# Kernel tuning notes

Hardware: AMD Instinct MI355X
Metric: run time of the kernel (lower is better)

## Reference

```python
import jax, jax.numpy as jnp
import numpy as np

B, S, D = 4, 2048, 256


def setup_inputs() -> dict:
    key = jax.random.key(0)
    ks = jax.random.split(key, 8)
    context = jax.random.normal(ks[0], (B, S, D), dtype=jnp.float32)
    eos_mask = jax.random.randint(ks[1], (B, S, S), 0, 2, dtype=jnp.int32)
    prior = jax.random.uniform(ks[2], (B, S, S), dtype=jnp.float32)
    Wq = jax.random.normal(ks[3], (D, D), dtype=jnp.float32) * 0.02
    bq = jnp.zeros((D,), dtype=jnp.float32)
    Wk = jax.random.normal(ks[4], (D, D), dtype=jnp.float32) * 0.02
    bk = jnp.zeros((D,), dtype=jnp.float32)
    ln_a = jnp.ones((D,), dtype=jnp.float32)
    ln_b = jnp.zeros((D,), dtype=jnp.float32)
    return {"context": context, "prior": prior, "Wq": Wq, "bq": bq,
            "Wk": Wk, "bk": bk, "ln_a": ln_a, "ln_b": ln_b,
            "eos_mask": eos_mask}


def reference(context, prior, Wq, bq, Wk, bk, ln_a, ln_b, eos_mask):
    seq = context.shape[1]
    # LayerNorm (torch: unbiased std, eps added to std)
    mean = context.mean(axis=-1, keepdims=True)
    std = jnp.std(context, axis=-1, ddof=1, keepdims=True)
    x = ln_a * (context - mean) / (std + 1e-6) + ln_b

    idx = jnp.arange(seq)
    diff = idx[None, :] - idx[:, None]
    a = diff == 1                      # superdiagonal
    offdiag = jnp.abs(diff) == 1       # a + c (super + sub diagonal)
    eye = diff == 0                    # b
    tri = jnp.triu(jnp.ones((seq, seq), dtype=jnp.float32))

    # mask = eos_mask & (a + c)  (precedence: & binds looser than +)
    mask = jnp.bitwise_and(eos_mask, offdiag.astype(jnp.int32))

    # torch Linear: y = x @ W.T + b
    query = x @ Wq.T + bq
    key = x @ Wk.T + bk
    scores = jnp.einsum('bqd,bkd->bqk', query, key) / 256.0
    scores = jnp.where(mask == 0, -1e9, scores)
    neibor = jax.nn.softmax(scores, axis=-1)
    neibor = jnp.sqrt(neibor * neibor.transpose(0, 2, 1) + 1e-9)
    neibor = prior + (1.0 - prior) * neibor

    # log -> zero except superdiagonal -> triangular matmul -> exp
    t = jnp.where(a, jnp.log(neibor + 1e-9), 0.0) @ tri   # [B,S,S]
    g = jnp.exp(jnp.matmul(tri, t))                        # [B,S,S]
    strict_upper = jnp.logical_and(tri.astype(bool), jnp.logical_not(eye))
    g = jnp.where(strict_upper, g, 0.0)  # masked_fill(tri - b == 0, 0)
    g = g + g.transpose(0, 2, 1) + jnp.where(eye, neibor, 1e-9)
    return g
```

## Files before the change

kernel.cpp:

```cpp
#include <hip/hip_runtime.h>
#include <math.h>

#define SS 2048
#define DD 256
#define NB 4
#define NR (NB * SS)

__global__ __launch_bounds__(256) void prep_kernel(
    const float* __restrict__ Wq, const float* __restrict__ Wk,
    const float* __restrict__ bq, float* __restrict__ A, float* __restrict__ u) {
    int t = threadIdx.x;
    int d = blockIdx.x;
    if (d < DD) {
        float a0 = 0.f, a1 = 0.f, a2 = 0.f, a3 = 0.f;
        for (int i = 0; i < DD; i += 4) {
            a0 += Wq[(i + 0) * DD + d] * Wk[(i + 0) * DD + t];
            a1 += Wq[(i + 1) * DD + d] * Wk[(i + 1) * DD + t];
            a2 += Wq[(i + 2) * DD + d] * Wk[(i + 2) * DD + t];
            a3 += Wq[(i + 3) * DD + d] * Wk[(i + 3) * DD + t];
        }
        A[d * DD + t] = (a0 + a1) + (a2 + a3);
    } else {
        float a0 = 0.f, a1 = 0.f, a2 = 0.f, a3 = 0.f;
        for (int i = 0; i < DD; i += 4) {
            a0 += Wk[(i + 0) * DD + t] * bq[i + 0];
            a1 += Wk[(i + 1) * DD + t] * bq[i + 1];
            a2 += Wk[(i + 2) * DD + t] * bq[i + 2];
            a3 += Wk[(i + 3) * DD + t] * bq[i + 3];
        }
        u[t] = (a0 + a1) + (a2 + a3);
    }
}

#define ROWS 16
#define BK 32
#define XP 260
#define FMA4(accv, a, bv) \
    accv.x += (a) * bv.x; accv.y += (a) * bv.y; \
    accv.z += (a) * bv.z; accv.w += (a) * bv.w;

__global__ __launch_bounds__(256) void gemm_score_kernel(
    const float4* __restrict__ ctx4, const float4* __restrict__ ln_a4,
    const float4* __restrict__ ln_b4, const float* __restrict__ A,
    const float* __restrict__ u, const int* __restrict__ eos,
    float4* __restrict__ pvals) {
    __shared__ float Xn[ROWS + 2][XP];
    __shared__ float As[BK][256];
    int tid = threadIdx.x;
    int lane = tid & 63;
    int wave = tid >> 6;
    int row0 = blockIdx.x * ROWS;
    const float4* A4 = (const float4*)A;

    float4 ga = ln_a4[lane], gb = ln_b4[lane];
    for (int rr = wave; rr < ROWS + 2; rr += 4) {
        int g = row0 - 1 + rr;
        g = (g < 0) ? 0 : (g > NR - 1 ? NR - 1 : g);
        float4 v = ctx4[(size_t)g * 64 + lane];
        float s = v.x + v.y + v.z + v.w;
#pragma unroll
        for (int off = 32; off > 0; off >>= 1) s += __shfl_xor(s, off, 64);
        float mean = s * (1.0f / 256.0f);
        float4 dd = make_float4(v.x - mean, v.y - mean, v.z - mean, v.w - mean);
        float s2 = dd.x * dd.x + dd.y * dd.y + dd.z * dd.z + dd.w * dd.w;
#pragma unroll
        for (int off = 32; off > 0; off >>= 1) s2 += __shfl_xor(s2, off, 64);
        float inv = 1.0f / (sqrtf(s2 * (1.0f / 255.0f)) + 1e-6f);
        float* xr = &Xn[rr][lane * 4];
        xr[0] = ga.x * dd.x * inv + gb.x;
        xr[1] = ga.y * dd.y * inv + gb.y;
        xr[2] = ga.z * dd.z * inv + gb.z;
        xr[3] = ga.w * dd.w * inv + gb.w;
    }

    int tx = tid & 15, ty = tid >> 4;
    float4 acc[4] = {};
    const float* xr0 = &Xn[1 + ty][0];
    for (int k0 = 0; k0 < DD; k0 += BK) {
#pragma unroll
        for (int q = 0; q < 8; q++) {
            int f4 = q * 256 + tid;
            int k = f4 >> 6, c4 = f4 & 63;
            *(float4*)&As[k][c4 * 4] = A4[(size_t)(k0 + k) * 64 + c4];
        }
        __syncthreads();
#pragma unroll
        for (int k = 0; k < BK; k++) {
            float a0 = xr0[k0 + k];
            float4 b0 = *(const float4*)&As[k][tx * 4];
            float4 b1 = *(const float4*)&As[k][tx * 4 + 64];
            float4 b2 = *(const float4*)&As[k][tx * 4 + 128];
            float4 b3 = *(const float4*)&As[k][tx * 4 + 192];
            FMA4(acc[0], a0, b0) FMA4(acc[1], a0, b1)
            FMA4(acc[2], a0, b2) FMA4(acc[3], a0, b3)
        }
        __syncthreads();
    }

    const float4* u4 = (const float4*)u;
#pragma unroll
    for (int q = 0; q < 4; q++) {
        float4 uv = u4[q * 16 + tx];
        acc[q].x += uv.x; acc[q].y += uv.y; acc[q].z += uv.z; acc[q].w += uv.w;
    }
    {
        int li = 1 + ty;
        int r = row0 + ty;
        int s = r & (SS - 1), b = r >> 11;
        bool has_n = (s < SS - 1), has_p = (s > 0);
        float fn = has_n ? 1.0f : 0.0f, fp = has_p ? 1.0f : 0.0f;
        float partial = 0.0f;
#pragma unroll
        for (int q = 0; q < 4; q++) {
            int c = q * 64 + tx * 4;
            float wx = fn * Xn[li + 1][c + 0] - fp * Xn[li - 1][c + 0];
            float wy = fn * Xn[li + 1][c + 1] - fp * Xn[li - 1][c + 1];
            float wz = fn * Xn[li + 1][c + 2] - fp * Xn[li - 1][c + 2];
            float ww = fn * Xn[li + 1][c + 3] - fp * Xn[li - 1][c + 3];
            partial += acc[q].x * wx + acc[q].y * wy
                     + acc[q].z * wz + acc[q].w * ww;
        }
#pragma unroll
        for (int off = 8; off > 0; off >>= 1) partial += __shfl_xor(partial, off, 64);
        if (tx == 0) {
            size_t base = (size_t)b * SS * SS + (size_t)s * SS;
            bool mn = has_n && (eos[base + s + 1] != 0);
            bool mp = has_p && (eos[base + s - 1] != 0);
            float pn, pp, pd;
            if (mn && mp) {
                float d = partial * (1.0f / 256.0f);
                pn = 1.0f / (1.0f + __expf(-d));
                pp = 1.0f - pn;
                pd = 0.0f;
            } else if (mn) { pn = 1.0f; pp = 0.0f; pd = 0.0f; }
            else if (mp)   { pn = 0.0f; pp = 1.0f; pd = 0.0f; }
            else           { pn = pp = pd = (1.0f / 2048.0f); }
            pvals[r] = make_float4(pn, pp, pd, 0.0f);
        }
    }
}

__global__ __launch_bounds__(256) void scan_kernel(
    const float4* __restrict__ pvals, const float* __restrict__ prior,
    float* __restrict__ P) {
    int b = blockIdx.x, t = threadIdx.x;
    int base_s = t * 8;
    double loc[8];
    double run = 0.0;
#pragma unroll
    for (int i = 0; i < 8; i++) {
        loc[i] = run;
        int s = base_s + i;
        float lv = 0.0f;
        if (s < SS - 1) {
            int r = b * SS + s;
            float4 pv = pvals[r];
            float4 pv1 = pvals[r + 1];
            float ns = sqrtf(pv.x * pv1.y + 1e-9f);
            float pr = prior[(size_t)b * SS * SS + (size_t)s * SS + s + 1];
            float neib = pr + (1.0f - pr) * ns;
            lv = logf(neib + 1e-9f);
        }
        run += (double)lv;
    }
    int lane = t & 63, wave = t >> 6;
    double v = run;
#pragma unroll
    for (int off = 1; off < 64; off <<= 1) {
        double uu = __shfl_up(v, off, 64);
        if (lane >= off) v += uu;
    }
    __shared__ double wsum[4];
    if (lane == 63) wsum[wave] = v;
    __syncthreads();
    double woff = 0.0;
    for (int w = 0; w < wave; w++) woff += wsum[w];
    double texcl = woff + (v - run);
#pragma unroll
    for (int i = 0; i < 8; i++)
        P[b * SS + base_s + i] = (float)(texcl + loc[i]);
}

__global__ __launch_bounds__(256) void fill_kernel(
    const float* __restrict__ P, const float4* __restrict__ pvals,
    const float* __restrict__ prior, float* __restrict__ out) {
    int blk = blockIdx.x;
    int i = blk & (SS - 1), b = blk >> 11;
    int t = threadIdx.x;
    __shared__ float shPi, shDv;
    if (t == 0) {
        shPi = P[blk];
        float pd = pvals[blk].z;
        float prd = prior[(size_t)b * SS * SS + (size_t)i * SS + i];
        shDv = prd + (1.0f - prd) * sqrtf(pd * pd + 1e-9f);
    }
    __syncthreads();
    float Pi = shPi, dv = shDv;
    const float* Pb = P + b * SS;
    size_t outbase = (size_t)blk * SS;
    float4 pj0 = *(const float4*)(Pb + t * 8);
    float4 pj1 = *(const float4*)(Pb + t * 8 + 4);
    float pj[8] = {pj0.x, pj0.y, pj0.z, pj0.w, pj1.x, pj1.y, pj1.z, pj1.w};
    float res[8];
#pragma unroll
    for (int k = 0; k < 8; k++) {
        int j = t * 8 + k;
        float d = (j > i) ? (pj[k] - Pi) : (Pi - pj[k]);
        float val = __expf(d) + 1e-9f;
        res[k] = (j == i) ? dv : val;
    }
    *(float4*)(out + outbase + t * 8) = make_float4(res[0], res[1], res[2], res[3]);
    *(float4*)(out + outbase + t * 8 + 4) = make_float4(res[4], res[5], res[6], res[7]);
}

extern "C" void kernel_launch(void* const* d_in, const int* in_sizes, int n_in,
                              void* d_out, int out_size, void* d_ws, size_t ws_size,
                              hipStream_t stream) {
    const float* context = (const float*)d_in[0];
    const float* prior   = (const float*)d_in[1];
    const float* Wq      = (const float*)d_in[2];
    const float* bq      = (const float*)d_in[3];
    const float* Wk      = (const float*)d_in[4];
    const float* ln_a    = (const float*)d_in[6];
    const float* ln_b    = (const float*)d_in[7];
    const int*   eos     = (const int*)d_in[8];
    float* out = (float*)d_out;

    float* ws = (float*)d_ws;
    float* A     = ws;
    float* u     = ws + 65536;
    float4* pv   = (float4*)(ws + 65792);
    float* P     = ws + 98560;

    prep_kernel<<<DD + 1, 256, 0, stream>>>(Wq, Wk, bq, A, u);
    gemm_score_kernel<<<NR / ROWS, 256, 0, stream>>>(
        (const float4*)context, (const float4*)ln_a, (const float4*)ln_b,
        A, u, eos, pv);
    scan_kernel<<<NB, 256, 0, stream>>>(pv, prior, P);
    fill_kernel<<<NR, 256, 0, stream>>>(P, pv, prior, out);
}
```

Baseline: 231.7 us.

## Remap GEMM tile so each wave owns 4 rows with register blocking

```diff
diff --git a/kernel.cpp b/kernel.cpp
--- a/kernel.cpp
+++ b/kernel.cpp
@@ -39,6 +39,24 @@
     accv.x += (a) * bv.x; accv.y += (a) * bv.y; \
     accv.z += (a) * bv.z; accv.w += (a) * bv.w;
 
+#define LOADG(g, av, b) \
+    av[0] = *(const float4*)&Xn[rbase + 0][k0 + (g) * 4]; \
+    av[1] = *(const float4*)&Xn[rbase + 1][k0 + (g) * 4]; \
+    av[2] = *(const float4*)&Xn[rbase + 2][k0 + (g) * 4]; \
+    av[3] = *(const float4*)&Xn[rbase + 3][k0 + (g) * 4]; \
+    b[0] = As4[((g) * 4 + 0) * 64 + lane]; \
+    b[1] = As4[((g) * 4 + 1) * 64 + lane]; \
+    b[2] = As4[((g) * 4 + 2) * 64 + lane]; \
+    b[3] = As4[((g) * 4 + 3) * 64 + lane];
+
+#define FMAG_J(av, bj, comp) \
+    FMA4(acc[0], av[0].comp, bj) FMA4(acc[1], av[1].comp, bj) \
+    FMA4(acc[2], av[2].comp, bj) FMA4(acc[3], av[3].comp, bj)
+
+#define FMAG(av, b) \
+    FMAG_J(av, b[0], x) FMAG_J(av, b[1], y) \
+    FMAG_J(av, b[2], z) FMAG_J(av, b[3], w)
+
 __global__ __launch_bounds__(256) void gemm_score_kernel(
     const float4* __restrict__ ctx4, const float4* __restrict__ ln_a4,
     const float4* __restrict__ ln_b4, const float* __restrict__ A,
@@ -73,9 +91,9 @@
         xr[3] = ga.w * dd.w * inv + gb.w;
     }
 
-    int tx = tid & 15, ty = tid >> 4;
     float4 acc[4] = {};
-    const float* xr0 = &Xn[1 + ty][0];
+    const float4* As4 = (const float4*)As;
+    int rbase = 1 + wave * 4;
     for (int k0 = 0; k0 < DD; k0 += BK) {
 #pragma unroll
         for (int q = 0; q < 8; q++) {
@@ -84,59 +102,68 @@
             *(float4*)&As[k][c4 * 4] = A4[(size_t)(k0 + k) * 64 + c4];
         }
         __syncthreads();
-#pragma unroll
-        for (int k = 0; k < BK; k++) {
-            float a0 = xr0[k0 + k];
-            float4 b0 = *(const float4*)&As[k][tx * 4];
-            float4 b1 = *(const float4*)&As[k][tx * 4 + 64];
-            float4 b2 = *(const float4*)&As[k][tx * 4 + 128];
-            float4 b3 = *(const float4*)&As[k][tx * 4 + 192];
-            FMA4(acc[0], a0, b0) FMA4(acc[1], a0, b1)
-            FMA4(acc[2], a0, b2) FMA4(acc[3], a0, b3)
+        {
+            float4 av0[4], b0[4], av1[4], b1[4];
+            LOADG(0, av0, b0)
+#pragma unroll
+            for (int g = 0; g < 3; g++) {
+                LOADG(2 * g + 1, av1, b1)
+                FMAG(av0, b0)
+                LOADG(2 * g + 2, av0, b0)
+                FMAG(av1, b1)
+            }
+            LOADG(7, av1, b1)
+            FMAG(av0, b0)
+            FMAG(av1, b1)
         }
         __syncthreads();
     }
 
-    const float4* u4 = (const float4*)u;
-#pragma unroll
-    for (int q = 0; q < 4; q++) {
-        float4 uv = u4[q * 16 + tx];
-        acc[q].x += uv.x; acc[q].y += uv.y; acc[q].z += uv.z; acc[q].w += uv.w;
-    }
     {
-        int li = 1 + ty;
-        int r = row0 + ty;
+        float4 uv = ((const float4*)u)[lane];
+#pragma unroll
+        for (int i = 0; i < 4; i++) {
+            acc[i].x += uv.x; acc[i].y += uv.y;
+            acc[i].z += uv.z; acc[i].w += uv.w;
+        }
+    }
+    float myp = 0.0f;
+#pragma unroll
+    for (int i = 0; i < 4; i++) {
+        int li = rbase + i;
+        int r = row0 + wave * 4 + i;
+        int s = r & (SS - 1);
+        float fn = (s < SS - 1) ? 1.0f : 0.0f;
+        float fp = (s > 0) ? 1.0f : 0.0f;
+        float4 n1 = *(const float4*)&Xn[li + 1][lane * 4];
+        float4 p1 = *(const float4*)&Xn[li - 1][lane * 4];
+        float partial =
+            acc[i].x * (fn * n1.x - fp * p1.x) +
+            acc[i].y * (fn * n1.y - fp * p1.y) +
+            acc[i].z * (fn * n1.z - fp * p1.z) +
+            acc[i].w * (fn * n1.w - fp * p1.w);
+#pragma unroll
+        for (int off = 32; off > 0; off >>= 1)
+            partial += __shfl_xor(partial, off, 64);
+        myp = (lane == i) ? partial : myp;
+    }
+    if (lane < 4) {
+        int r = row0 + wave * 4 + lane;
         int s = r & (SS - 1), b = r >> 11;
         bool has_n = (s < SS - 1), has_p = (s > 0);
-        float fn = has_n ? 1.0f : 0.0f, fp = has_p ? 1.0f : 0.0f;
-        float partial = 0.0f;
-#pragma unroll
-        for (int q = 0; q < 4; q++) {
-            int c = q * 64 + tx * 4;
-            float wx = fn * Xn[li + 1][c + 0] - fp * Xn[li - 1][c + 0];
-            float wy = fn * Xn[li + 1][c + 1] - fp * Xn[li - 1][c + 1];
-            float wz = fn * Xn[li + 1][c + 2] - fp * Xn[li - 1][c + 2];
-            float ww = fn * Xn[li + 1][c + 3] - fp * Xn[li - 1][c + 3];
-            partial += acc[q].x * wx + acc[q].y * wy
-                     + acc[q].z * wz + acc[q].w * ww;
-        }
-#pragma unroll
-        for (int off = 8; off > 0; off >>= 1) partial += __shfl_xor(partial, off, 64);
-        if (tx == 0) {
-            size_t base = (size_t)b * SS * SS + (size_t)s * SS;
-            bool mn = has_n && (eos[base + s + 1] != 0);
-            bool mp = has_p && (eos[base + s - 1] != 0);
-            float pn, pp, pd;
-            if (mn && mp) {
-                float d = partial * (1.0f / 256.0f);
-                pn = 1.0f / (1.0f + __expf(-d));
-                pp = 1.0f - pn;
-                pd = 0.0f;
-            } else if (mn) { pn = 1.0f; pp = 0.0f; pd = 0.0f; }
-            else if (mp)   { pn = 0.0f; pp = 1.0f; pd = 0.0f; }
-            else           { pn = pp = pd = (1.0f / 2048.0f); }
-            pvals[r] = make_float4(pn, pp, pd, 0.0f);
-        }
+        size_t base = (size_t)b * SS * SS + (size_t)s * SS;
+        bool mn = has_n && (eos[base + s + 1] != 0);
+        bool mp = has_p && (eos[base + s - 1] != 0);
+        float pn, pp, pd;
+        if (mn && mp) {
+            float d = myp * (1.0f / 256.0f);
+            pn = 1.0f / (1.0f + __expf(-d));
+            pp = 1.0f - pn;
+            pd = 0.0f;
+        } else if (mn) { pn = 1.0f; pp = 0.0f; pd = 0.0f; }
+        else if (mp)   { pn = 0.0f; pp = 1.0f; pd = 0.0f; }
+        else           { pn = pp = pd = (1.0f / 2048.0f); }
+        pvals[r] = make_float4(pn, pp, pd, 0.0f);
     }
 }
 
```

Measured after the change: 221.4 us. -4.5%, faster.
